# Performance work log

Measured on AMD Instinct MI355X. Metric: run time of the kernel, lower is better.

## Reference

```python
import jax, jax.numpy as jnp
import numpy as np

B, S, D = 2, 2048, 2048
H, DN, DR, DV, R = 16, 128, 64, 128, 512
EPS = 1e-6


def rmsnorm(x, g, eps=EPS):
    var = jnp.mean(x * x, axis=-1, keepdims=True)
    return x * jax.lax.rsqrt(var + eps) * g


def apply_rope(x, freqs):
    # x: [B,S,H,DR], freqs: [S, DR//2] angles. Complex-pair (interleaved) rotation.
    b, s, h, d = x.shape
    xp = x.reshape(b, s, h, d // 2, 2)
    xr, xi = xp[..., 0], xp[..., 1]
    cos = jnp.cos(freqs)[None, :, None, :]
    sin = jnp.sin(freqs)[None, :, None, :]
    outr = xr * cos - xi * sin
    outi = xr * sin + xi * cos
    return jnp.stack([outr, outi], axis=-1).reshape(b, s, h, d)


def setup_inputs() -> dict:
    key = jax.random.key(0)
    ks = jax.random.split(key, 8)
    x = jax.random.normal(ks[0], (B, S, D), dtype=jnp.float32)
    # RoPE angles: pos * inv_freq, standard theta=10000
    inv_freq = 1.0 / (10000.0 ** (np.arange(0, DR, 2, dtype=np.float32) / DR))
    freqs = jnp.asarray(np.arange(S, dtype=np.float32)[:, None] * inv_freq[None, :])
    sc = lambda fan_in: 1.0 / np.sqrt(fan_in)
    # weights stored [in, out] so forward is x @ W
    w_kv = jax.random.normal(ks[1], (D, R), dtype=jnp.float32) * sc(D)
    g_kv = jnp.ones((R,), dtype=jnp.float32)
    w_k = jax.random.normal(ks[2], (R, H * (DN + DR)), dtype=jnp.float32) * sc(R)
    w_v = jax.random.normal(ks[3], (R, H * DV), dtype=jnp.float32) * sc(R)
    w_qn = jax.random.normal(ks[4], (D, H * DN), dtype=jnp.float32) * sc(D)
    w_qr = jax.random.normal(ks[5], (D, H * DR), dtype=jnp.float32) * sc(D)
    w_o = jax.random.normal(ks[6], (H * DV, D), dtype=jnp.float32) * sc(H * DV)
    return {"x": x, "freqs": freqs, "w_kv": w_kv, "g_kv": g_kv, "w_k": w_k,
            "w_v": w_v, "w_qn": w_qn, "w_qr": w_qr, "w_o": w_o}


def reference(x, freqs, w_kv, g_kv, w_k, w_v, w_qn, w_qr, w_o):
    b, s, _ = x.shape
    # latent KV compression + RMSNorm
    kv = rmsnorm(x @ w_kv, g_kv)                       # [B,S,R]
    k_full = (kv @ w_k).reshape(b, s, H, DN + DR)      # [B,S,H,192]
    k_nope, k_rope = k_full[..., :DN], k_full[..., DN:]
    v = (kv @ w_v).reshape(b, s, H, DV)                # [B,S,H,DV]
    q_nope = (x @ w_qn).reshape(b, s, H, DN)
    q_rope = (x @ w_qr).reshape(b, s, H, DR)
    q_rope = apply_rope(q_rope, freqs)
    k_rope = apply_rope(k_rope, freqs)
    q = jnp.concatenate([q_nope, q_rope], axis=-1)     # [B,S,H,192]
    k = jnp.concatenate([k_nope, k_rope], axis=-1)
    scale = 1.0 / np.sqrt(DN + DR)
    scores = jnp.einsum('bshd,bthd->bhst', q, k) * scale  # [B,H,S,S]
    causal = jnp.tril(jnp.ones((s, s), dtype=bool))
    scores = jnp.where(causal[None, None], scores, jnp.float32(-1e30))
    attn = jax.nn.softmax(scores, axis=-1)
    out = jnp.einsum('bhst,bthd->bshd', attn, v).reshape(b, s, H * DV)
    return out @ w_o                                   # [B,S,D]
```

## Files before the change

### kernel.cpp

```cpp
#include <hip/hip_runtime.h>

typedef __bf16 bf16_t;
typedef bf16_t bf16x8 __attribute__((ext_vector_type(8)));
typedef bf16_t bf16x4v __attribute__((ext_vector_type(4)));
typedef float f32x4 __attribute__((ext_vector_type(4)));

#define GLDS16(g, l) __builtin_amdgcn_global_load_lds( \
    (const __attribute__((address_space(1))) void*)(g), \
    (__attribute__((address_space(3))) void*)(l), 16, 0, 0)

#define BB 2
#define SEQ 2048
#define DMODEL 2048
#define RDIM 512
#define NH 16
#define DNOPE 128
#define DROPE 64
#define DVDIM 128
#define MROWS 4096
#define DQK 192


__global__ __launch_bounds__(256) void cast_x_kernel(const float* __restrict__ x,
                                                     bf16_t* __restrict__ xb) {
    int idx = blockIdx.x * 256 + threadIdx.x;
    float4 v = ((const float4*)x)[idx];
    bf16x4v o;
    o[0] = (bf16_t)v.x; o[1] = (bf16_t)v.y; o[2] = (bf16_t)v.z; o[3] = (bf16_t)v.w;
    ((bf16x4v*)xb)[idx] = o;
}

__global__ __launch_bounds__(256) void wtrans_kernel(const float* __restrict__ W,
                                                     bf16_t* __restrict__ WT,
                                                     int K, int N) {
    __shared__ float t[32][33];
    int n0 = blockIdx.x * 32, k0 = blockIdx.y * 32;
    int tx = threadIdx.x & 31, ty = threadIdx.x >> 5;
    #pragma unroll
    for (int i = 0; i < 4; ++i)
        t[ty + i*8][tx] = W[(size_t)(k0 + ty + i*8) * N + n0 + tx];
    __syncthreads();
    #pragma unroll
    for (int i = 0; i < 4; ++i)
        WT[(size_t)(n0 + ty + i*8) * K + k0 + tx] = (bf16_t)t[tx][ty + i*8];
}

__global__ __launch_bounds__(256) void rope_table_kernel(const float* __restrict__ freqs,
                                                         float* __restrict__ costab,
                                                         float* __restrict__ sintab) {
    int idx = blockIdx.x * 256 + threadIdx.x;
    float f = freqs[idx];
    costab[idx] = cosf(f);
    sintab[idx] = sinf(f);
}

__global__ __launch_bounds__(256) void rmsnorm_kernel(const float* __restrict__ kvf,
                                                      const float* __restrict__ gkv,
                                                      bf16_t* __restrict__ kvb) {
    int m = blockIdx.x;
    int tid = threadIdx.x;
    const float* rowp = kvf + (size_t)m * RDIM;
    float2 v = *(const float2*)(rowp + tid * 2);
    float ss = v.x * v.x + v.y * v.y;
    #pragma unroll
    for (int d = 1; d < 64; d <<= 1) ss += __shfl_xor(ss, d, 64);
    __shared__ float red[4];
    if ((tid & 63) == 0) red[tid >> 6] = ss;
    __syncthreads();
    float tot = red[0] + red[1] + red[2] + red[3];
    float scale = rsqrtf(tot * (1.0f / RDIM) + 1e-6f);
    bf16_t* orow = kvb + (size_t)m * RDIM;
    orow[tid*2]     = (bf16_t)(v.x * scale * gkv[tid*2]);
    orow[tid*2 + 1] = (bf16_t)(v.y * scale * gkv[tid*2 + 1]);
}


template<typename OutT, int EPI>
__global__ __launch_bounds__(256, 2) void gemm_bt(const bf16_t* __restrict__ A,
                                                  const bf16_t* __restrict__ Bt,
                                                  OutT* __restrict__ C,
                                                  int M, int N, int K,
                                                  const float* __restrict__ costab,
                                                  const float* __restrict__ sintab,
                                                  bf16_t* __restrict__ C2) {
    __shared__ __align__(16) char ldsA[128 * 128];
    __shared__ __align__(16) char ldsB[128 * 128];
    int tid = threadIdx.x;
    int lane = tid & 63, wave = tid >> 6;
    int n0 = blockIdx.x * 128, m0 = blockIdx.y * 128;
    int wr = wave >> 1, wc = wave & 1;
    int g = lane >> 4, c = lane & 15;
    f32x4 acc[4][4] = {};

    int srow = tid >> 3;
    int sch = tid & 7;

    int nkt = K >> 6;
    for (int kt = 0; kt < nkt; ++kt) {
        int k0 = kt << 6;
        #pragma unroll
        for (int j = 0; j < 4; ++j) {
            int row = j * 32 + srow;
            int csrc = sch ^ (row & 7);
            const char* gA = (const char*)(A + (size_t)(m0 + row) * K + k0) + csrc * 16;
            const char* gB = (const char*)(Bt + (size_t)(n0 + row) * K + k0) + csrc * 16;
            char* lA = ldsA + j * 4096 + wave * 1024;
            char* lB = ldsB + j * 4096 + wave * 1024;
            GLDS16(gA, lA);
            GLDS16(gB, lB);
        }
        __syncthreads();
        #pragma unroll
        for (int kk = 0; kk < 2; ++kk) {
            int kb = kk * 64 + g * 16;
            bf16x8 aF[4], bF[4];
            #pragma unroll
            for (int m = 0; m < 4; ++m) {
                int row = wr * 64 + m * 16 + c;
                aF[m] = *(const bf16x8*)(ldsA + row * 128 + (kb ^ ((row & 7) << 4)));
            }
            #pragma unroll
            for (int n = 0; n < 4; ++n) {
                int row = wc * 64 + n * 16 + c;
                bF[n] = *(const bf16x8*)(ldsB + row * 128 + (kb ^ ((row & 7) << 4)));
            }
            #pragma unroll
            for (int m = 0; m < 4; ++m)
                #pragma unroll
                for (int n = 0; n < 4; ++n)
                    acc[m][n] = __builtin_amdgcn_mfma_f32_16x16x32_bf16(aF[m], bF[n], acc[m][n], 0, 0, 0);
        }
        __syncthreads();
    }
    #pragma unroll
    for (int m = 0; m < 4; ++m) {
        int grow0 = m0 + wr * 64 + m * 16 + g * 4;
        #pragma unroll
        for (int n = 0; n < 4; ++n) {
            int gcol = n0 + wc * 64 + n * 16 + c;
            if (EPI == 3) {
                if (gcol < 512) {
                    #pragma unroll
                    for (int i = 0; i < 4; ++i)
                        C[(size_t)(grow0 + i) * 512 + gcol] = (OutT)acc[m][n][i];
                } else {
                    int qcol = gcol - 512;
                    if (qcol >= 2048) {
                        int j = ((qcol - 2048) & 63) >> 1;
                        bool even = (c & 1) == 0;
                        #pragma unroll
                        for (int i = 0; i < 4; ++i) {
                            float v = acc[m][n][i];
                            float pv = __shfl_xor(v, 1, 64);
                            int s = (grow0 + i) & (SEQ - 1);
                            float cs = costab[s * 32 + j], sn = sintab[s * 32 + j];
                            float o = even ? (v * cs - pv * sn) : (pv * sn + v * cs);
                            C2[(size_t)(grow0 + i) * 3072 + qcol] = (bf16_t)o;
                        }
                    } else {
                        #pragma unroll
                        for (int i = 0; i < 4; ++i)
                            C2[(size_t)(grow0 + i) * 3072 + qcol] = (bf16_t)acc[m][n][i];
                    }
                }
            } else {
                bool rope = false;
                int j = 0;
                if (EPI == 1) {
                    rope = (gcol < 3072) && ((gcol % 192) >= 128);
                    j = ((gcol % 192) - 128) >> 1;
                } else if (EPI == 2) {
                    rope = (gcol >= 2048);
                    j = ((gcol - 2048) & 63) >> 1;
                }
                if (EPI != 0 && rope) {
                    bool even = (c & 1) == 0;
                    #pragma unroll
                    for (int i = 0; i < 4; ++i) {
                        float v = acc[m][n][i];
                        float pv = __shfl_xor(v, 1, 64);
                        int s = (grow0 + i) & (SEQ - 1);
                        float cs = costab[s * 32 + j], sn = sintab[s * 32 + j];
                        float o = even ? (v * cs - pv * sn) : (pv * sn + v * cs);
                        C[(size_t)(grow0 + i) * N + gcol] = (OutT)o;
                    }
                } else {
                    #pragma unroll
                    for (int i = 0; i < 4; ++i)
                        C[(size_t)(grow0 + i) * N + gcol] = (OutT)acc[m][n][i];
                }
            }
        }
    }
}

__global__ __launch_bounds__(256) void pack_v_kernel(const bf16_t* __restrict__ kvout,
                                                     bf16_t* __restrict__ vt) {
    __shared__ bf16_t t[64][144];
    int blk = blockIdx.x;
    int bh = blk >> 5, st = blk & 31;
    int s0 = st * 64;
    int b = bh >> 4, h = bh & 15;
    int tid = threadIdx.x;
    #pragma unroll
    for (int i = 0; i < 4; ++i) {
        int id = i * 256 + tid;
        int row = id >> 4, ch = id & 15;
        bf16x8 v = *(const bf16x8*)(kvout + (size_t)(b * SEQ + s0 + row) * 5120 + 3072 + h * 128 + ch * 8);
        *(bf16x8*)&t[row][ch * 8] = v;
    }
    __syncthreads();
    #pragma unroll
    for (int i = 0; i < 4; ++i) {
        int id = i * 256 + tid;
        int dv = id >> 3, sc = id & 7;
        bf16x8 v;
        #pragma unroll
        for (int jj = 0; jj < 8; ++jj) v[jj] = t[sc * 8 + jj][dv];
        *(bf16x8*)(vt + ((size_t)bh * 128 + dv) * SEQ + s0 + sc * 8) = v;
    }
}


__global__ __launch_bounds__(512, 2) void attn_kernel(const bf16_t* __restrict__ Qf,
                                                      const bf16_t* __restrict__ KV,
                                                      const bf16_t* __restrict__ VT,
                                                      bf16_t* __restrict__ O) {
    __shared__ __align__(16) char ldsK[3 * 64 * 384];
    __shared__ __align__(16) char ldsV[3 * 128 * 128];
    __shared__ __align__(16) char ldsP[8 * 16 * 176];
    int tid = threadIdx.x, lane = tid & 63, wave = tid >> 6;
    int g = lane >> 4, c = lane & 15;

    int bid = blockIdx.x;
    int xcd = bid & 7, r = bid >> 3;
    int bh = xcd * 4 + (r & 3);
    int p = r >> 2;
    int b = bh >> 4, h = bh & 15;

    const bf16_t* Kb = KV + (size_t)b * SEQ * 5120 + h * DQK;
    const bf16_t* Vb = VT + (size_t)bh * 128 * SEQ;
    char* ldsPw = ldsP + wave * (16 * 176);

    size_t soff[3];
    #pragma unroll
    for (int i2 = 0; i2 < 3; ++i2) {
        int id = i2 * 512 + tid;
        int row = id / 24, ch = id - row * 24;
        soff[i2] = (size_t)row * 10240 + (ch ^ (row & 7)) * 16;
    }
    size_t voff[2];
    #pragma unroll
    for (int i2 = 0; i2 < 2; ++i2) {
        int id = i2 * 512 + tid;
        int row = id >> 3, ch = id & 7;
        voff[i2] = (size_t)row * (SEQ * 2) + (ch ^ (row & 7)) * 16;
    }
    const float sc = 0.0721687836f * 1.44269504f;

    bf16x8 vones;
    #pragma unroll
    for (int j = 0; j < 8; ++j) vones[j] = (bf16_t)1.0f;

    auto stage = [&](int t, int buf) {
        const char* Kt = (const char*)(Kb + (size_t)t * 64 * 5120);
        #pragma unroll
        for (int i2 = 0; i2 < 3; ++i2)
            GLDS16(Kt + soff[i2], ldsK + buf * 24576 + i2 * 8192 + wave * 1024);
        const char* Vt = (const char*)Vb + (size_t)t * 128;
        #pragma unroll
        for (int i2 = 0; i2 < 2; ++i2)
            GLDS16(Vt + voff[i2], ldsV + buf * 16384 + i2 * 8192 + wave * 1024);
    };

    #pragma unroll 1
    for (int pass = 0; pass < 2; ++pass) {
        int qt = pass ? p : (15 - p);
        int q0 = qt * 128;
        int nt = 2 * qt + 2;
        int tdiag = 2 * qt + (wave >> 2);

        bf16x8 qf[6];
        {
            int qrow = q0 + wave * 16 + c;
            const bf16_t* qn = Qf + (size_t)(b * SEQ + qrow) * 3072 + h * DNOPE + g * 8;
            #pragma unroll
            for (int kk = 0; kk < 4; ++kk) qf[kk] = *(const bf16x8*)(qn + kk * 32);
            const bf16_t* qr = Qf + (size_t)(b * SEQ + qrow) * 3072 + 2048 + h * DROPE + g * 8;
            qf[4] = *(const bf16x8*)(qr);
            qf[5] = *(const bf16x8*)(qr + 32);
            #pragma unroll
            for (int kk = 0; kk < 6; ++kk)
                #pragma unroll
                for (int j = 0; j < 8; ++j)
                    qf[kk][j] = (bf16_t)((float)qf[kk][j] * sc);
        }
        float m_run[4];
        f32x4 accO[9] = {};
        #pragma unroll
        for (int i = 0; i < 4; ++i) m_run[i] = -3.0e38f;

        stage(0, 0);
        stage(1, 1);

        #pragma unroll 1
        for (int t = 0; t < nt; ++t) {
            int cur = t - (t / 3) * 3;
            if (t + 1 < nt) asm volatile("s_waitcnt vmcnt(5)" ::: "memory");
            else            asm volatile("s_waitcnt vmcnt(0)" ::: "memory");
            __builtin_amdgcn_s_barrier();
            __builtin_amdgcn_sched_barrier(0);
            asm volatile("" ::: "memory");
            if (t + 2 < nt) stage(t + 2, (t + 2) % 3);

            if (t <= tdiag) {
                bool diag = (t == tdiag);
                const char* ldsKc = ldsK + cur * 24576;
                const char* ldsVc = ldsV + cur * 16384;

                f32x4 accS[4] = {};
                __builtin_amdgcn_s_setprio(1);
                #pragma unroll
                for (int kk = 0; kk < 6; ++kk) {
                    int kb = kk * 64 + g * 16;
                    #pragma unroll
                    for (int n = 0; n < 4; ++n) {
                        int row = n * 16 + c;
                        bf16x8 kf = *(const bf16x8*)(ldsKc + row * 384 + (kb ^ ((row & 7) << 4)));
                        accS[n] = __builtin_amdgcn_mfma_f32_16x16x32_bf16(qf[kk], kf, accS[n], 0, 0, 0);
                    }
                }
                __builtin_amdgcn_s_setprio(0);

                if (diag) {
                    #pragma unroll
                    for (int n = 0; n < 4; ++n)
                        #pragma unroll
                        for (int i = 0; i < 4; ++i)
                            if (n * 16 + c > (wave & 3) * 16 + g * 4 + i) accS[n][i] = -1e30f;
                }
                float mx[4];
                #pragma unroll
                for (int i = 0; i < 4; ++i) {
                    float m2 = fmaxf(fmaxf(accS[0][i], accS[1][i]), fmaxf(accS[2][i], accS[3][i]));
                    #pragma unroll
                    for (int d = 1; d < 16; d <<= 1) m2 = fmaxf(m2, __shfl_xor(m2, d, 64));
                    mx[i] = m2;
                }
                bool nore = __all((mx[0] <= m_run[0] + 8.f) & (mx[1] <= m_run[1] + 8.f) &
                                  (mx[2] <= m_run[2] + 8.f) & (mx[3] <= m_run[3] + 8.f));
                if (nore) {
                    #pragma unroll
                    for (int i = 0; i < 4; ++i)
                        #pragma unroll
                        for (int n = 0; n < 4; ++n)
                            accS[n][i] = exp2f(accS[n][i] - m_run[i]);
                } else {
                    #pragma unroll
                    for (int i = 0; i < 4; ++i) {
                        float mnew = fmaxf(m_run[i], mx[i]);
                        float alpha = exp2f(m_run[i] - mnew);
                        m_run[i] = mnew;
                        #pragma unroll
                        for (int n = 0; n < 4; ++n)
                            accS[n][i] = exp2f(accS[n][i] - mnew);
                        #pragma unroll
                        for (int n = 0; n < 9; ++n) accO[n][i] *= alpha;
                    }
                }
                #pragma unroll
                for (int n = 0; n < 4; ++n)
                    #pragma unroll
                    for (int i = 0; i < 4; ++i)
                        *(bf16_t*)(ldsPw + (g * 4 + i) * 176 + (n * 16 + c) * 2) = (bf16_t)accS[n][i];
                bf16x8 pf0 = *(const bf16x8*)(ldsPw + c * 176 + g * 16);
                bf16x8 pf1 = *(const bf16x8*)(ldsPw + c * 176 + 64 + g * 16);

                __builtin_amdgcn_s_setprio(1);
                #pragma unroll
                for (int n = 0; n < 8; ++n) {
                    int row = n * 16 + c;
                    bf16x8 vf0 = *(const bf16x8*)(ldsVc + row * 128 + ((g * 16) ^ ((c & 7) << 4)));
                    bf16x8 vf1 = *(const bf16x8*)(ldsVc + row * 128 + ((64 + g * 16) ^ ((c & 7) << 4)));
                    accO[n] = __builtin_amdgcn_mfma_f32_16x16x32_bf16(pf0, vf0, accO[n], 0, 0, 0);
                    accO[n] = __builtin_amdgcn_mfma_f32_16x16x32_bf16(pf1, vf1, accO[n], 0, 0, 0);
                }
                accO[8] = __builtin_amdgcn_mfma_f32_16x16x32_bf16(pf0, vones, accO[8], 0, 0, 0);
                accO[8] = __builtin_amdgcn_mfma_f32_16x16x32_bf16(pf1, vones, accO[8], 0, 0, 0);
                __builtin_amdgcn_s_setprio(0);
            }
        }
        float inv_l[4];
        #pragma unroll
        for (int i = 0; i < 4; ++i) inv_l[i] = 1.0f / accO[8][i];
        #pragma unroll
        for (int n = 0; n < 8; ++n) {
            int gcol = h * 128 + n * 16 + c;
            #pragma unroll
            for (int i = 0; i < 4; ++i) {
                int mrow = b * SEQ + q0 + wave * 16 + g * 4 + i;
                O[(size_t)mrow * 2048 + gcol] = (bf16_t)(accO[n][i] * inv_l[i]);
            }
        }
        __syncthreads();
    }
}


extern "C" void kernel_launch(void* const* d_in, const int* in_sizes, int n_in,
                              void* d_out, int out_size, void* d_ws, size_t ws_size,
                              hipStream_t stream) {
    const float* x     = (const float*)d_in[0];
    const float* freqs = (const float*)d_in[1];
    const float* w_kv  = (const float*)d_in[2];
    const float* g_kv  = (const float*)d_in[3];
    const float* w_k   = (const float*)d_in[4];
    const float* w_v   = (const float*)d_in[5];
    const float* w_qn  = (const float*)d_in[6];
    const float* w_qr  = (const float*)d_in[7];
    const float* w_o   = (const float*)d_in[8];
    float* out = (float*)d_out;

    char* ws = (char*)d_ws;
    size_t off = 0;
    auto alloc = [&](size_t bytes) { char* p = ws + off; off += (bytes + 255) & ~(size_t)255; return p; };
    bf16_t* xb     = (bf16_t*)alloc((size_t)MROWS * DMODEL * 2);
    bf16_t* wqkT   = (bf16_t*)alloc((size_t)3584 * DMODEL * 2);
    bf16_t* wkvwT  = (bf16_t*)alloc((size_t)5120 * RDIM * 2);
    bf16_t* woT    = (bf16_t*)alloc((size_t)DMODEL * DMODEL * 2);
    float*  kvf    = (float*) alloc((size_t)MROWS * RDIM * 4);
    bf16_t* kvb    = (bf16_t*)alloc((size_t)MROWS * RDIM * 2);
    bf16_t* kvout  = (bf16_t*)alloc((size_t)MROWS * 5120 * 2);
    bf16_t* qfull  = (bf16_t*)alloc((size_t)MROWS * 3072 * 2);
    bf16_t* vt     = (bf16_t*)alloc((size_t)32 * 128 * SEQ * 2);
    bf16_t* attno  = (bf16_t*)alloc((size_t)MROWS * 2048 * 2);
    float*  costab = (float*) alloc((size_t)SEQ * 32 * 4);
    float*  sintab = (float*) alloc((size_t)SEQ * 32 * 4);

    cast_x_kernel<<<(MROWS * DMODEL / 4) / 256, 256, 0, stream>>>(x, xb);
    wtrans_kernel<<<dim3(RDIM / 32, DMODEL / 32), 256, 0, stream>>>(w_kv, wqkT, DMODEL, RDIM);
    wtrans_kernel<<<dim3(2048 / 32, DMODEL / 32), 256, 0, stream>>>(w_qn, wqkT + (size_t)512 * DMODEL, DMODEL, 2048);
    wtrans_kernel<<<dim3(1024 / 32, DMODEL / 32), 256, 0, stream>>>(w_qr, wqkT + (size_t)2560 * DMODEL, DMODEL, 1024);
    wtrans_kernel<<<dim3(3072 / 32, RDIM / 32), 256, 0, stream>>>(w_k, wkvwT, RDIM, 3072);
    wtrans_kernel<<<dim3(2048 / 32, RDIM / 32), 256, 0, stream>>>(w_v, wkvwT + (size_t)3072 * RDIM, RDIM, 2048);
    wtrans_kernel<<<dim3(2048 / 32, DMODEL / 32), 256, 0, stream>>>(w_o, woT, DMODEL, 2048);
    rope_table_kernel<<<(SEQ * 32) / 256, 256, 0, stream>>>(freqs, costab, sintab);

    gemm_bt<float, 3><<<dim3(3584 / 128, MROWS / 128), 256, 0, stream>>>(
        xb, wqkT, kvf, MROWS, 3584, DMODEL, costab, sintab, qfull);
    rmsnorm_kernel<<<MROWS, 256, 0, stream>>>(kvf, g_kv, kvb);
    gemm_bt<bf16_t, 1><<<dim3(5120 / 128, MROWS / 128), 256, 0, stream>>>(
        kvb, wkvwT, kvout, MROWS, 5120, RDIM, costab, sintab, nullptr);

    pack_v_kernel<<<32 * 32, 256, 0, stream>>>(kvout, vt);

    attn_kernel<<<256, 512, 0, stream>>>(qfull, kvout, vt, attno);

    gemm_bt<float, 0><<<dim3(2048 / 128, MROWS / 128), 256, 0, stream>>>(
        attno, woT, out, MROWS, 2048, DMODEL, nullptr, nullptr, nullptr);
}
```

Baseline: 304.4 us.

## Fuse V transpose into KV GEMM epilogue, merge weight transposes, defer row-max shuffles

The KV up-projection GEMM epilogue now writes V directly in the transposed [b,h,dv,s] layout, so the separate pack_v kernel and its read/write of V go away. The K buffer shrinks to stride 3072. The six weight-transpose launches are merged into three multi-source launches, and GEMM launch bounds are raised to 3 blocks per CU. In attention, the cross-lane row-max shuffle reduction now runs only on the rescale path, since the fast-path check uses per-lane maxima under __all. The higher occupancy bound may force register spills, and the transposed V writes are 4-element strided stores that coalesce poorly.

Measured after the change: 277.3 us (median of 3 runs). -8.9%, faster.

```diff
diff --git a/kernel.cpp b/kernel.cpp
--- a/kernel.cpp
+++ b/kernel.cpp
@@ -19,6 +19,7 @@
 #define DVDIM 128
 #define MROWS 4096
 #define DQK 192
+#define KSTRIDE 3072
 
 
 __global__ __launch_bounds__(256) void cast_x_kernel(const float* __restrict__ x,
@@ -30,15 +31,23 @@
     ((bf16x4v*)xb)[idx] = o;
 }
 
-__global__ __launch_bounds__(256) void wtrans_kernel(const float* __restrict__ W,
-                                                     bf16_t* __restrict__ WT,
-                                                     int K, int N) {
+__global__ __launch_bounds__(256) void wtrans3_kernel(const float* __restrict__ W0,
+                                                      const float* __restrict__ W1,
+                                                      const float* __restrict__ W2,
+                                                      int N0, int N1, int N2,
+                                                      int b1, int b2,
+                                                      bf16_t* __restrict__ WT, int K) {
     __shared__ float t[32][33];
     int n0 = blockIdx.x * 32, k0 = blockIdx.y * 32;
+    const float* W; int Nsrc, cb;
+    if (n0 < b1)      { W = W0; Nsrc = N0; cb = 0; }
+    else if (n0 < b2) { W = W1; Nsrc = N1; cb = b1; }
+    else              { W = W2; Nsrc = N2; cb = b2; }
+    int col = n0 - cb;
     int tx = threadIdx.x & 31, ty = threadIdx.x >> 5;
     #pragma unroll
     for (int i = 0; i < 4; ++i)
-        t[ty + i*8][tx] = W[(size_t)(k0 + ty + i*8) * N + n0 + tx];
+        t[ty + i*8][tx] = W[(size_t)(k0 + ty + i*8) * Nsrc + col + tx];
     __syncthreads();
     #pragma unroll
     for (int i = 0; i < 4; ++i)
@@ -76,7 +85,7 @@
 
 
 template<typename OutT, int EPI>
-__global__ __launch_bounds__(256, 2) void gemm_bt(const bf16_t* __restrict__ A,
+__global__ __launch_bounds__(256, 3) void gemm_bt(const bf16_t* __restrict__ A,
                                                   const bf16_t* __restrict__ Bt,
                                                   OutT* __restrict__ C,
                                                   int M, int N, int K,
@@ -138,7 +147,36 @@
         #pragma unroll
         for (int n = 0; n < 4; ++n) {
             int gcol = n0 + wc * 64 + n * 16 + c;
-            if (EPI == 3) {
+            if (EPI == 1) {
+                if (gcol < 3072) {
+                    bool rope = (gcol % 192) >= 128;
+                    if (rope) {
+                        int j = ((gcol % 192) - 128) >> 1;
+                        bool even = (c & 1) == 0;
+                        #pragma unroll
+                        for (int i = 0; i < 4; ++i) {
+                            float v = acc[m][n][i];
+                            float pv = __shfl_xor(v, 1, 64);
+                            int s = (grow0 + i) & (SEQ - 1);
+                            float cs = costab[s * 32 + j], sn = sintab[s * 32 + j];
+                            float o = even ? (v * cs - pv * sn) : (pv * sn + v * cs);
+                            C[(size_t)(grow0 + i) * KSTRIDE + gcol] = (OutT)o;
+                        }
+                    } else {
+                        #pragma unroll
+                        for (int i = 0; i < 4; ++i)
+                            C[(size_t)(grow0 + i) * KSTRIDE + gcol] = (OutT)acc[m][n][i];
+                    }
+                } else {
+                    int vcol = gcol - 3072;
+                    int hh = vcol >> 7, dv = vcol & 127;
+                    int bb = grow0 >> 11, s = grow0 & (SEQ - 1);
+                    bf16x4v o;
+                    #pragma unroll
+                    for (int i = 0; i < 4; ++i) o[i] = (bf16_t)acc[m][n][i];
+                    *(bf16x4v*)(C2 + ((size_t)(bb * NH + hh) * 128 + dv) * SEQ + s) = o;
+                }
+            } else if (EPI == 3) {
                 if (gcol < 512) {
                     #pragma unroll
                     for (int i = 0; i < 4; ++i)
@@ -164,60 +202,11 @@
                     }
                 }
             } else {
-                bool rope = false;
-                int j = 0;
-                if (EPI == 1) {
-                    rope = (gcol < 3072) && ((gcol % 192) >= 128);
-                    j = ((gcol % 192) - 128) >> 1;
-                } else if (EPI == 2) {
-                    rope = (gcol >= 2048);
-                    j = ((gcol - 2048) & 63) >> 1;
-                }
-                if (EPI != 0 && rope) {
-                    bool even = (c & 1) == 0;
-                    #pragma unroll
-                    for (int i = 0; i < 4; ++i) {
-                        float v = acc[m][n][i];
-                        float pv = __shfl_xor(v, 1, 64);
-                        int s = (grow0 + i) & (SEQ - 1);
-                        float cs = costab[s * 32 + j], sn = sintab[s * 32 + j];
-                        float o = even ? (v * cs - pv * sn) : (pv * sn + v * cs);
-                        C[(size_t)(grow0 + i) * N + gcol] = (OutT)o;
-                    }
-                } else {
-                    #pragma unroll
-                    for (int i = 0; i < 4; ++i)
-                        C[(size_t)(grow0 + i) * N + gcol] = (OutT)acc[m][n][i];
-                }
+                #pragma unroll
+                for (int i = 0; i < 4; ++i)
+                    C[(size_t)(grow0 + i) * N + gcol] = (OutT)acc[m][n][i];
             }
         }
-    }
-}
-
-__global__ __launch_bounds__(256) void pack_v_kernel(const bf16_t* __restrict__ kvout,
-                                                     bf16_t* __restrict__ vt) {
-    __shared__ bf16_t t[64][144];
-    int blk = blockIdx.x;
-    int bh = blk >> 5, st = blk & 31;
-    int s0 = st * 64;
-    int b = bh >> 4, h = bh & 15;
-    int tid = threadIdx.x;
-    #pragma unroll
-    for (int i = 0; i < 4; ++i) {
-        int id = i * 256 + tid;
-        int row = id >> 4, ch = id & 15;
-        bf16x8 v = *(const bf16x8*)(kvout + (size_t)(b * SEQ + s0 + row) * 5120 + 3072 + h * 128 + ch * 8);
-        *(bf16x8*)&t[row][ch * 8] = v;
-    }
-    __syncthreads();
-    #pragma unroll
-    for (int i = 0; i < 4; ++i) {
-        int id = i * 256 + tid;
-        int dv = id >> 3, sc = id & 7;
-        bf16x8 v;
-        #pragma unroll
-        for (int jj = 0; jj < 8; ++jj) v[jj] = t[sc * 8 + jj][dv];
-        *(bf16x8*)(vt + ((size_t)bh * 128 + dv) * SEQ + s0 + sc * 8) = v;
     }
 }
 
@@ -238,7 +227,7 @@
     int p = r >> 2;
     int b = bh >> 4, h = bh & 15;
 
-    const bf16_t* Kb = KV + (size_t)b * SEQ * 5120 + h * DQK;
+    const bf16_t* Kb = KV + (size_t)b * SEQ * KSTRIDE + h * DQK;
     const bf16_t* Vb = VT + (size_t)bh * 128 * SEQ;
     char* ldsPw = ldsP + wave * (16 * 176);
 
@@ -247,7 +236,7 @@
     for (int i2 = 0; i2 < 3; ++i2) {
         int id = i2 * 512 + tid;
         int row = id / 24, ch = id - row * 24;
-        soff[i2] = (size_t)row * 10240 + (ch ^ (row & 7)) * 16;
+        soff[i2] = (size_t)row * (KSTRIDE * 2) + (ch ^ (row & 7)) * 16;
     }
     size_t voff[2];
     #pragma unroll
@@ -263,7 +252,7 @@
     for (int j = 0; j < 8; ++j) vones[j] = (bf16_t)1.0f;
 
     auto stage = [&](int t, int buf) {
-        const char* Kt = (const char*)(Kb + (size_t)t * 64 * 5120);
+        const char* Kt = (const char*)Kb + (size_t)t * (64 * KSTRIDE * 2);
         #pragma unroll
         for (int i2 = 0; i2 < 3; ++i2)
             GLDS16(Kt + soff[i2], ldsK + buf * 24576 + i2 * 8192 + wave * 1024);
@@ -339,17 +328,13 @@
                         for (int i = 0; i < 4; ++i)
                             if (n * 16 + c > (wave & 3) * 16 + g * 4 + i) accS[n][i] = -1e30f;
                 }
-                float mx[4];
-                #pragma unroll
-                for (int i = 0; i < 4; ++i) {
-                    float m2 = fmaxf(fmaxf(accS[0][i], accS[1][i]), fmaxf(accS[2][i], accS[3][i]));
-                    #pragma unroll
-                    for (int d = 1; d < 16; d <<= 1) m2 = fmaxf(m2, __shfl_xor(m2, d, 64));
-                    mx[i] = m2;
-                }
-                bool nore = __all((mx[0] <= m_run[0] + 8.f) & (mx[1] <= m_run[1] + 8.f) &
-                                  (mx[2] <= m_run[2] + 8.f) & (mx[3] <= m_run[3] + 8.f));
-                if (nore) {
+                float mloc[4];
+                #pragma unroll
+                for (int i = 0; i < 4; ++i)
+                    mloc[i] = fmaxf(fmaxf(accS[0][i], accS[1][i]), fmaxf(accS[2][i], accS[3][i]));
+                bool cheap = __all((mloc[0] <= m_run[0] + 8.f) & (mloc[1] <= m_run[1] + 8.f) &
+                                   (mloc[2] <= m_run[2] + 8.f) & (mloc[3] <= m_run[3] + 8.f));
+                if (cheap) {
                     #pragma unroll
                     for (int i = 0; i < 4; ++i)
                         #pragma unroll
@@ -358,7 +343,10 @@
                 } else {
                     #pragma unroll
                     for (int i = 0; i < 4; ++i) {
-                        float mnew = fmaxf(m_run[i], mx[i]);
+                        float m2 = mloc[i];
+                        #pragma unroll
+                        for (int d = 1; d < 16; d <<= 1) m2 = fmaxf(m2, __shfl_xor(m2, d, 64));
+                        float mnew = fmaxf(m_run[i], m2);
                         float alpha = exp2f(m_run[i] - mnew);
                         m_run[i] = mnew;
                         #pragma unroll
@@ -430,7 +418,7 @@
     bf16_t* woT    = (bf16_t*)alloc((size_t)DMODEL * DMODEL * 2);
     float*  kvf    = (float*) alloc((size_t)MROWS * RDIM * 4);
     bf16_t* kvb    = (bf16_t*)alloc((size_t)MROWS * RDIM * 2);
-    bf16_t* kvout  = (bf16_t*)alloc((size_t)MROWS * 5120 * 2);
+    bf16_t* kvout  = (bf16_t*)alloc((size_t)MROWS * KSTRIDE * 2);
     bf16_t* qfull  = (bf16_t*)alloc((size_t)MROWS * 3072 * 2);
     bf16_t* vt     = (bf16_t*)alloc((size_t)32 * 128 * SEQ * 2);
     bf16_t* attno  = (bf16_t*)alloc((size_t)MROWS * 2048 * 2);
@@ -438,21 +426,19 @@
     float*  sintab = (float*) alloc((size_t)SEQ * 32 * 4);
 
     cast_x_kernel<<<(MROWS * DMODEL / 4) / 256, 256, 0, stream>>>(x, xb);
-    wtrans_kernel<<<dim3(RDIM / 32, DMODEL / 32), 256, 0, stream>>>(w_kv, wqkT, DMODEL, RDIM);
-    wtrans_kernel<<<dim3(2048 / 32, DMODEL / 32), 256, 0, stream>>>(w_qn, wqkT + (size_t)512 * DMODEL, DMODEL, 2048);
-    wtrans_kernel<<<dim3(1024 / 32, DMODEL / 32), 256, 0, stream>>>(w_qr, wqkT + (size_t)2560 * DMODEL, DMODEL, 1024);
-    wtrans_kernel<<<dim3(3072 / 32, RDIM / 32), 256, 0, stream>>>(w_k, wkvwT, RDIM, 3072);
-    wtrans_kernel<<<dim3(2048 / 32, RDIM / 32), 256, 0, stream>>>(w_v, wkvwT + (size_t)3072 * RDIM, RDIM, 2048);
-    wtrans_kernel<<<dim3(2048 / 32, DMODEL / 32), 256, 0, stream>>>(w_o, woT, DMODEL, 2048);
+    wtrans3_kernel<<<dim3(3584 / 32, DMODEL / 32), 256, 0, stream>>>(
+        w_kv, w_qn, w_qr, 512, 2048, 1024, 512, 2560, wqkT, DMODEL);
+    wtrans3_kernel<<<dim3(5120 / 32, RDIM / 32), 256, 0, stream>>>(
+        w_k, w_v, w_v, 3072, 2048, 2048, 3072, 5120, wkvwT, RDIM);
+    wtrans3_kernel<<<dim3(2048 / 32, DMODEL / 32), 256, 0, stream>>>(
+        w_o, w_o, w_o, 2048, 2048, 2048, 2048, 4096, woT, DMODEL);
     rope_table_kernel<<<(SEQ * 32) / 256, 256, 0, stream>>>(freqs, costab, sintab);
 
     gemm_bt<float, 3><<<dim3(3584 / 128, MROWS / 128), 256, 0, stream>>>(
         xb, wqkT, kvf, MROWS, 3584, DMODEL, costab, sintab, qfull);
     rmsnorm_kernel<<<MROWS, 256, 0, stream>>>(kvf, g_kv, kvb);
     gemm_bt<bf16_t, 1><<<dim3(5120 / 128, MROWS / 128), 256, 0, stream>>>(
-        kvb, wkvwT, kvout, MROWS, 5120, RDIM, costab, sintab, nullptr);
-
-    pack_v_kernel<<<32 * 32, 256, 0, stream>>>(kvout, vt);
+        kvb, wkvwT, kvout, MROWS, 5120, RDIM, costab, sintab, vt);
 
     attn_kernel<<<256, 512, 0, stream>>>(qfull, kvout, vt, attno);
 
```
